# Kernel tuning notes

Measured on AMD Instinct MI355X. Metric: run time of the kernel, lower is better.

The kernel has to match this reference:

```python
import jax, jax.numpy as jnp
import numpy as np

B, T, M, D, L = 8, 4096, 32768, 128, 3  # L = ebm_GNN_layer_num - 1


def _lin(x, W, b):
    return x @ W + b


def setup_inputs() -> dict:
    key = jax.random.key(0)
    ks = jax.random.split(key, 24)
    s = 0.05
    inp = {
        "x_1st": jax.random.normal(ks[0], (B, T, 2, D), dtype=jnp.float32),
        "x_2nd": jax.random.normal(ks[1], (B, M, 4, D), dtype=jnp.float32),
        "A_causal": jax.random.uniform(ks[2], (B, 1, M), dtype=jnp.float32),
        "edge": jax.random.randint(ks[3], (2, M), 0, T, dtype=jnp.int64),
        # per-layer node/edge weights (stacked over L layers)
        "node_W": jax.random.normal(ks[4], (L, D, D)) * s,
        "node_b": jnp.zeros((L, D)),
        "mlp_W": jax.random.normal(ks[5], (L, D, D)) * s,
        "mlp_b": jnp.zeros((L, D)),
        "edgeL_W": jax.random.normal(ks[6], (L, D, D)) * s,
        "edgeL_b": jnp.zeros((L, D)),
        # node readout MLP: D -> 2D -> D -> 1
        "nro_W1": jax.random.normal(ks[7], (D, 2 * D)) * s, "nro_b1": jnp.zeros((2 * D,)),
        "nro_W2": jax.random.normal(ks[8], (2 * D, D)) * s, "nro_b2": jnp.zeros((D,)),
        "nro_W3": jax.random.normal(ks[9], (D, 1)) * s, "nro_b3": jnp.zeros((1,)),
        # edge readout MLP
        "ero_W1": jax.random.normal(ks[10], (D, 2 * D)) * s, "ero_b1": jnp.zeros((2 * D,)),
        "ero_W2": jax.random.normal(ks[11], (2 * D, D)) * s, "ero_b2": jnp.zeros((D,)),
        "ero_W3": jax.random.normal(ks[12], (D, 1)) * s, "ero_b3": jnp.zeros((1,)),
    }
    return inp


def reference(x_1st, x_2nd, A_causal, node_W, node_b, mlp_W, mlp_b,
              edgeL_W, edgeL_b, nro_W1, nro_b1, nro_W2, nro_b2, nro_W3, nro_b3,
              ero_W1, ero_b1, ero_W2, ero_b2, ero_W3, ero_b3, edge):
    ni = jnp.array([0, 0, 1, 1])  # node_i_indice
    nj = jnp.array([0, 1, 0, 1])  # node_j_indice
    e0, e1 = edge[0], edge[1]
    a = A_causal[:, 0, :, None, None]  # (B, M, 1, 1)
    xn, xe = x_1st, x_2nd
    for i in range(L):
        # --- node layer: gather -> mask-multiply -> scatter_add -> linear ---
        msg = xn[:, e1] * a                          # (B, M, 2, D)
        upd = jnp.zeros_like(xn).at[:, e0].add(msg)  # (B, T, 2, D)
        xn_new = _lin(xn + upd, node_W[i], node_b[i])
        # --- edge layer (uses updated node features, as in torch forward) ---
        ei = xn_new[:, e0][:, :, ni]                 # (B, M, 4, D)
        ej = xn_new[:, e1][:, :, nj]                 # (B, M, 4, D)
        xe_new = _lin(xe + _lin(ei + ej, mlp_W[i], mlp_b[i]), edgeL_W[i], edgeL_b[i])
        if i < L - 1:
            xn_new = jax.nn.relu(xn_new)
            xe_new = jax.nn.relu(xe_new)
        xn, xe = xn_new, xe_new
    # readouts (dropout=0, concat=False)
    h_node = _lin(jax.nn.relu(_lin(jax.nn.relu(_lin(xn, nro_W1, nro_b1)), nro_W2, nro_b2)), nro_W3, nro_b3)[..., 0]
    h_edge = _lin(jax.nn.relu(_lin(jax.nn.relu(_lin(xe, ero_W1, ero_b1)), ero_W2, ero_b2)), ero_W3, ero_b3)[..., 0]
    return h_node, h_edge  # (B,T,2), (B,M,4)
```

## Files before the change

kernel.cpp:

```cpp
#include <hip/hip_runtime.h>

#define NB 8
#define NT 4096
#define NM 32768
#define ND 128

typedef __attribute__((ext_vector_type(8))) short bf16x8;
typedef __attribute__((ext_vector_type(4))) float f32x4;
typedef __attribute__((ext_vector_type(4))) unsigned int u32x4;
typedef __attribute__((ext_vector_type(2))) unsigned int u32x2;

#define MFMA(a,b,c) __builtin_amdgcn_mfma_f32_16x16x32_bf16(a,b,c,0,0,0)

__device__ __forceinline__ unsigned short f2bf(float x) {
  unsigned u = __float_as_uint(x);
  u += 0x7FFFu + ((u >> 16) & 1u);
  return (unsigned short)(u >> 16);
}
__device__ __forceinline__ float bf2f(unsigned short h) {
  return __uint_as_float(((unsigned)h) << 16);
}
__device__ __forceinline__ u32x2 pack4bf(float a, float b, float c, float d) {
  u32x2 r;
  r[0] = ((unsigned)f2bf(b) << 16) | f2bf(a);
  r[1] = ((unsigned)f2bf(d) << 16) | f2bf(c);
  return r;
}

__device__ __forceinline__ bf16x8 ldsFrag(const char* lds, int row, int kByte, int rowStride) {
  return *(const bf16x8*)(lds + ((row * rowStride + kByte) ^ ((row & 7) << 4)));
}

__global__ __launch_bounds__(256) void k_prep(
    const float* __restrict__ W, char* __restrict__ dst,
    int K, int N, int khShift, int perShift, int total)
{
  int i = blockIdx.x * 256 + threadIdx.x;
  if (i >= total) return;
  int m  = i >> perShift;
  int j  = i & ((1 << perShift) - 1);
  int n  = j >> khShift;
  int kh = j & ((1 << khShift) - 1);
  int k0 = kh << 3;
  const float* Wm = W + (size_t)m * K * N;
  char* dm = dst + (size_t)m * K * N * 2;
  unsigned short tmp[8];
  #pragma unroll
  for (int jj = 0; jj < 8; ++jj) tmp[jj] = f2bf(Wm[(k0 + jj) * N + n]);
  *(u32x4*)(dm + ((n * K * 2 + k0 * 2) ^ ((n & 7) << 4))) = *(u32x4*)tmp;
}

__global__ __launch_bounds__(256) void k_csr_count(const int* __restrict__ edge, int* deg) {
  int m = blockIdx.x * 256 + threadIdx.x;
  if (m < NM) atomicAdd(&deg[edge[m]], 1);
}
__global__ __launch_bounds__(64) void k_csr_scan(const int* __restrict__ deg,
                                                 int* __restrict__ off, int* __restrict__ cursor) {
  __shared__ int partial[64];
  int t = threadIdx.x;
  int base = t * 64;
  int sum = 0;
  for (int i = 0; i < 64; ++i) sum += deg[base + i];
  partial[t] = sum;
  __syncthreads();
  if (t == 0) {
    int run = 0;
    for (int i = 0; i < 64; ++i) { int v = partial[i]; partial[i] = run; run += v; }
  }
  __syncthreads();
  int run = partial[t];
  for (int i = 0; i < 64; ++i) {
    off[base + i] = run; cursor[base + i] = run;
    run += deg[base + i];
  }
  if (t == 63) off[NT] = NM;
}
__global__ __launch_bounds__(256) void k_csr_fill(const int* __restrict__ edge,
                                                  int* cursor, int* __restrict__ csr) {
  int m = blockIdx.x * 256 + threadIdx.x;
  if (m < NM) { int pos = atomicAdd(&cursor[edge[m]], 1); csr[pos] = m; }
}
__global__ __launch_bounds__(256) void k_csr_sort(const int* __restrict__ off, int* __restrict__ csr) {
  int n = blockIdx.x * 256 + threadIdx.x;
  if (n < NT) {
    int s = off[n], e = off[n + 1];
    for (int i = s + 1; i < e; ++i) {
      int v = csr[i]; int j = i - 1;
      while (j >= s && csr[j] > v) { csr[j + 1] = csr[j]; --j; }
      csr[j + 1] = v;
    }
  }
}

__global__ __launch_bounds__(256, 4) void k_node(
    const float* __restrict__ xnIn, float* __restrict__ xnOut,
    const float* __restrict__ A, const int* __restrict__ edge,
    const int* __restrict__ off, const int* __restrict__ csr,
    const char* __restrict__ WImg, const float* __restrict__ bias,
    int doReluIn, int nTiles)
{
  __shared__ __align__(16) char WT[128 * 256];
  __shared__ __align__(16) char xs[32 * 256];
  const int t = threadIdx.x;
  {
    const u32x4* s = (const u32x4*)WImg;
    u32x4* d = (u32x4*)WT;
    for (int i = t; i < 2048; i += 256) d[i] = s[i];
  }
  const int w   = t >> 6;
  const int l   = t & 63;
  const int l15 = l & 15;
  const int lg  = l >> 4;
  float4 bv4[2];
  #pragma unroll
  for (int fc = 0; fc < 2; ++fc)
    bv4[fc] = *(const float4*)(bias + w * 32 + fc * 16 + lg * 4);
  const int gr = t >> 3;
  const int c0 = (t & 7) << 4;
  __syncthreads();

  for (int tile = blockIdx.x; tile < nTiles; tile += gridDim.x) {
    const int rowBase = tile << 5;
    {
      const int grow = rowBase + gr;
      const int ch   = grow & 1;
      const int node = (grow >> 1) & (NT - 1);
      const int b    = grow >> 13;
      f32x4 acc[4];
      {
        const float4* xr = (const float4*)(xnIn + (size_t)grow * ND + c0);
        #pragma unroll
        for (int q = 0; q < 4; ++q) {
          float4 v = xr[q];
          if (doReluIn) {
            v.x = fmaxf(v.x, 0.f); v.y = fmaxf(v.y, 0.f);
            v.z = fmaxf(v.z, 0.f); v.w = fmaxf(v.w, 0.f);
          }
          acc[q] = (f32x4){v.x, v.y, v.z, v.w};
        }
      }
      const int s = off[node], e = off[node + 1];
      for (int p = s; p < e; ++p) {
        int m = csr[p];
        float a = A[b * NM + m];
        int e1 = edge[NM + m];
        const float4* src = (const float4*)(xnIn + (size_t)(((b * NT + e1) << 1) + ch) * ND + c0);
        #pragma unroll
        for (int q = 0; q < 4; ++q) {
          float4 v = src[q];
          if (doReluIn) {
            v.x = fmaxf(v.x, 0.f); v.y = fmaxf(v.y, 0.f);
            v.z = fmaxf(v.z, 0.f); v.w = fmaxf(v.w, 0.f);
          }
          acc[q][0] = fmaf(a, v.x, acc[q][0]);
          acc[q][1] = fmaf(a, v.y, acc[q][1]);
          acc[q][2] = fmaf(a, v.z, acc[q][2]);
          acc[q][3] = fmaf(a, v.w, acc[q][3]);
        }
      }
      unsigned short tmp[8];
      #pragma unroll
      for (int q = 0; q < 2; ++q)
        #pragma unroll
        for (int j = 0; j < 4; ++j) tmp[q * 4 + j] = f2bf(acc[q][j]);
      *(u32x4*)(xs + ((gr * 256 + c0 * 2) ^ ((gr & 7) << 4))) = *(u32x4*)tmp;
      #pragma unroll
      for (int q = 0; q < 2; ++q)
        #pragma unroll
        for (int j = 0; j < 4; ++j) tmp[q * 4 + j] = f2bf(acc[2 + q][j]);
      *(u32x4*)(xs + ((gr * 256 + c0 * 2 + 16) ^ ((gr & 7) << 4))) = *(u32x4*)tmp;
    }
    __syncthreads();
    f32x4 acc2[2][2];
    #pragma unroll
    for (int fr = 0; fr < 2; ++fr)
      #pragma unroll
      for (int fc = 0; fc < 2; ++fc) acc2[fr][fc] = (f32x4){0.f, 0.f, 0.f, 0.f};
    #pragma unroll
    for (int ks = 0; ks < 4; ++ks) {
      int kb = ks * 64 + lg * 16;
      bf16x8 b0 = ldsFrag(WT, w * 32 + l15,      kb, 256);
      bf16x8 b1 = ldsFrag(WT, w * 32 + 16 + l15, kb, 256);
      bf16x8 a0 = ldsFrag(xs, l15,      kb, 256);
      bf16x8 a1 = ldsFrag(xs, 16 + l15, kb, 256);
      acc2[0][0] = MFMA(b0, a0, acc2[0][0]);
      acc2[0][1] = MFMA(b1, a0, acc2[0][1]);
      acc2[1][0] = MFMA(b0, a1, acc2[1][0]);
      acc2[1][1] = MFMA(b1, a1, acc2[1][1]);
    }
    __syncthreads();
    #pragma unroll
    for (int fr = 0; fr < 2; ++fr)
      #pragma unroll
      for (int fc = 0; fc < 2; ++fc) {
        int row = rowBase + fr * 16 + l15;
        int col0 = w * 32 + fc * 16 + lg * 4;
        float4 o;
        o.x = acc2[fr][fc][0] + bv4[fc].x;
        o.y = acc2[fr][fc][1] + bv4[fc].y;
        o.z = acc2[fr][fc][2] + bv4[fc].z;
        o.w = acc2[fr][fc][3] + bv4[fc].w;
        *(float4*)&xnOut[(size_t)row * ND + col0] = o;
      }
  }
}

template<int IN_F32>
__global__ __launch_bounds__(512, 2) void k_edge_mfma(
    const float* __restrict__ xn,
    const float* __restrict__ xeInF, const unsigned short* __restrict__ xeInH,
    unsigned short* xeOut,
    const int* __restrict__ edge,
    const char* __restrict__ WmImg, const float* __restrict__ bm,
    const char* __restrict__ WeImg, const float* __restrict__ be,
    int doReluOut, int nTiles)
{
  __shared__ __align__(16) char sA[64 * 256];
  __shared__ __align__(16) char sB[64 * 256];
  const int t = threadIdx.x;
  const int w   = t >> 6;
  const int l   = t & 63;
  const int l15 = l & 15;
  const int lg  = l >> 4;
  const int rg2 = w >> 2;
  const int wc  = w & 3;
  bf16x8 wmf[4][2], wef[4][2];
  #pragma unroll
  for (int ks = 0; ks < 4; ++ks)
    #pragma unroll
    for (int fc = 0; fc < 2; ++fc) {
      int n = wc * 32 + fc * 16 + l15;
      int kb = ks * 64 + lg * 16;
      wmf[ks][fc] = *(const bf16x8*)(WmImg + ((n * 256 + kb) ^ ((n & 7) << 4)));
      wef[ks][fc] = *(const bf16x8*)(WeImg + ((n * 256 + kb) ^ ((n & 7) << 4)));
    }
  float4 bmv[2], bev[2];
  #pragma unroll
  for (int fc = 0; fc < 2; ++fc) {
    int col0 = wc * 32 + fc * 16 + lg * 4;
    bmv[fc] = *(const float4*)(bm + col0);
    bev[fc] = *(const float4*)(be + col0);
  }
  const int srow = t >> 3;

  for (int tile = blockIdx.x; tile < nTiles; tile += gridDim.x) {
    const int rowBase = tile << 6;
    {
      int grow = rowBase + srow;
      int cch = grow & 3;
      int m = (grow >> 2) & (NM - 1);
      int b = grow >> 17;
      int e0 = edge[m], e1 = edge[NM + m];
      const float4* p0 = (const float4*)(xn + (size_t)((b * NT + e0) * 2 + (cch >> 1)) * ND);
      const float4* p1 = (const float4*)(xn + (size_t)((b * NT + e1) * 2 + (cch & 1)) * ND);
      #pragma unroll
      for (int hh = 0; hh < 2; ++hh) {
        int h = (t & 7) + hh * 8;
        float4 a0 = p0[h * 2], a1 = p0[h * 2 + 1];
        float4 c0 = p1[h * 2], c1 = p1[h * 2 + 1];
        unsigned short tmp[8];
        tmp[0] = f2bf(a0.x + c0.x); tmp[1] = f2bf(a0.y + c0.y);
        tmp[2] = f2bf(a0.z + c0.z); tmp[3] = f2bf(a0.w + c0.w);
        tmp[4] = f2bf(a1.x + c1.x); tmp[5] = f2bf(a1.y + c1.y);
        tmp[6] = f2bf(a1.z + c1.z); tmp[7] = f2bf(a1.w + c1.w);
        *(u32x4*)(sA + ((srow * 256 + h * 16) ^ ((srow & 7) << 4))) = *(u32x4*)tmp;
      }
    }
    float4 xev[2][2];
    #pragma unroll
    for (int fr = 0; fr < 2; ++fr)
      #pragma unroll
      for (int fc = 0; fc < 2; ++fc) {
        int row = rowBase + rg2 * 32 + fr * 16 + l15;
        int col0 = wc * 32 + fc * 16 + lg * 4;
        if (IN_F32) {
          xev[fr][fc] = *(const float4*)(xeInF + (size_t)row * ND + col0);
        } else {
          ushort4 h4 = *(const ushort4*)(xeInH + (size_t)row * ND + col0);
          xev[fr][fc] = (float4){bf2f(h4.x), bf2f(h4.y), bf2f(h4.z), bf2f(h4.w)};
        }
      }
    __syncthreads();
    f32x4 acc[2][2];
    #pragma unroll
    for (int fr = 0; fr < 2; ++fr)
      #pragma unroll
      for (int fc = 0; fc < 2; ++fc) acc[fr][fc] = (f32x4){0.f, 0.f, 0.f, 0.f};
    #pragma unroll
    for (int ks = 0; ks < 4; ++ks) {
      int kb = ks * 64 + lg * 16;
      #pragma unroll
      for (int fr = 0; fr < 2; ++fr) {
        bf16x8 a = ldsFrag(sA, rg2 * 32 + fr * 16 + l15, kb, 256);
        acc[fr][0] = MFMA(wmf[ks][0], a, acc[fr][0]);
        acc[fr][1] = MFMA(wmf[ks][1], a, acc[fr][1]);
      }
    }
    #pragma unroll
    for (int fr = 0; fr < 2; ++fr)
      #pragma unroll
      for (int fc = 0; fc < 2; ++fc) {
        int row = rg2 * 32 + fr * 16 + l15;
        int kByte = (wc * 32 + fc * 16 + lg * 4) * 2;
        u32x2 pk = pack4bf(xev[fr][fc].x + acc[fr][fc][0] + bmv[fc].x,
                           xev[fr][fc].y + acc[fr][fc][1] + bmv[fc].y,
                           xev[fr][fc].z + acc[fr][fc][2] + bmv[fc].z,
                           xev[fr][fc].w + acc[fr][fc][3] + bmv[fc].w);
        *(u32x2*)(sB + ((row * 256 + kByte) ^ ((row & 7) << 4))) = pk;
      }
    __syncthreads();
    #pragma unroll
    for (int fr = 0; fr < 2; ++fr)
      #pragma unroll
      for (int fc = 0; fc < 2; ++fc) acc[fr][fc] = (f32x4){0.f, 0.f, 0.f, 0.f};
    #pragma unroll
    for (int ks = 0; ks < 4; ++ks) {
      int kb = ks * 64 + lg * 16;
      #pragma unroll
      for (int fr = 0; fr < 2; ++fr) {
        bf16x8 a = ldsFrag(sB, rg2 * 32 + fr * 16 + l15, kb, 256);
        acc[fr][0] = MFMA(wef[ks][0], a, acc[fr][0]);
        acc[fr][1] = MFMA(wef[ks][1], a, acc[fr][1]);
      }
    }
    #pragma unroll
    for (int fr = 0; fr < 2; ++fr)
      #pragma unroll
      for (int fc = 0; fc < 2; ++fc) {
        int row = rowBase + rg2 * 32 + fr * 16 + l15;
        int col0 = wc * 32 + fc * 16 + lg * 4;
        float o0 = acc[fr][fc][0] + bev[fc].x;
        float o1 = acc[fr][fc][1] + bev[fc].y;
        float o2 = acc[fr][fc][2] + bev[fc].z;
        float o3 = acc[fr][fc][3] + bev[fc].w;
        if (doReluOut) {
          o0 = fmaxf(o0, 0.f); o1 = fmaxf(o1, 0.f);
          o2 = fmaxf(o2, 0.f); o3 = fmaxf(o3, 0.f);
        }
        u32x2 pk = pack4bf(o0, o1, o2, o3);
        *(u32x2*)(xeOut + (size_t)row * ND + col0) = pk;
      }
  }
}

template<int INBF16>
__global__ __launch_bounds__(512, 2) void k_ro_fused(
    const float* __restrict__ inF, const unsigned short* __restrict__ inH,
    float* __restrict__ out, int nTiles,
    const char* __restrict__ W1Img, const float* __restrict__ b1,
    const char* __restrict__ W2Img, const float* __restrict__ b2,
    const float* __restrict__ W3, const float* __restrict__ b3)
{
  __shared__ __align__(16) char sA[64 * 256];
  __shared__ __align__(16) char h1[64 * 512];
  __shared__ float red[2][64][8];
  const int t = threadIdx.x;
  const int w   = t >> 6;
  const int l   = t & 63;
  const int l15 = l & 15;
  const int lg  = l >> 4;
  bf16x8 w1f[4][2];
  #pragma unroll
  for (int ks = 0; ks < 4; ++ks)
    #pragma unroll
    for (int fc = 0; fc < 2; ++fc) {
      int n = w * 32 + fc * 16 + l15;
      int kb = ks * 64 + lg * 16;
      w1f[ks][fc] = *(const bf16x8*)(W1Img + ((n * 256 + kb) ^ ((n & 7) << 4)));
    }
  bf16x8 w2f[8];
  #pragma unroll
  for (int ks = 0; ks < 8; ++ks) {
    int n = w * 16 + l15;
    int kb = ks * 64 + lg * 16;
    w2f[ks] = *(const bf16x8*)(W2Img + ((n * 512 + kb) ^ ((n & 7) << 4)));
  }
  float4 b1v[2];
  #pragma unroll
  for (int fc = 0; fc < 2; ++fc)
    b1v[fc] = *(const float4*)(b1 + w * 32 + fc * 16 + lg * 4);
  const float4 b2v = *(const float4*)(b2 + w * 16 + lg * 4);
  const float4 w3v = *(const float4*)(W3 + w * 16 + lg * 4);
  const float b3v = b3[0];
  const int srow  = t >> 3;
  const int sbyte = (t & 7) << 5;
  u32x4 pvH[2];
  int tile = blockIdx.x;
  if (tile < nTiles) {
    if (INBF16) {
      const char* p = (const char*)inH + (size_t)((tile << 6) + srow) * 256 + sbyte;
      pvH[0] = *(const u32x4*)p;
      pvH[1] = *(const u32x4*)(p + 16);
    } else {
      const float4* p = (const float4*)(inF + (size_t)((tile << 6) + srow) * ND + ((t & 7) << 4));
      unsigned short tmp[16];
      #pragma unroll
      for (int q = 0; q < 4; ++q) {
        float4 v = p[q];
        tmp[q * 4 + 0] = f2bf(v.x); tmp[q * 4 + 1] = f2bf(v.y);
        tmp[q * 4 + 2] = f2bf(v.z); tmp[q * 4 + 3] = f2bf(v.w);
      }
      pvH[0] = *(u32x4*)tmp; pvH[1] = *(u32x4*)(tmp + 8);
    }
  }

  int par = 0;
  int prevRow = -1;
  for (; tile < nTiles; tile += gridDim.x) {
    const int rowBase = tile << 6;
    *(u32x4*)(sA + ((srow * 256 + sbyte) ^ ((srow & 7) << 4))) = pvH[0];
    *(u32x4*)(sA + ((srow * 256 + sbyte + 16) ^ ((srow & 7) << 4))) = pvH[1];
    __syncthreads();
    if (prevRow >= 0 && t < 64) {
      float s = b3v;
      #pragma unroll
      for (int q = 0; q < 8; ++q) s += red[par ^ 1][t][q];
      out[prevRow + t] = s;
    }
    {
      int nt2 = tile + (int)gridDim.x;
      if (nt2 < nTiles) {
        if (INBF16) {
          const char* p = (const char*)inH + (size_t)((nt2 << 6) + srow) * 256 + sbyte;
          pvH[0] = *(const u32x4*)p;
          pvH[1] = *(const u32x4*)(p + 16);
        } else {
          const float4* p = (const float4*)(inF + (size_t)((nt2 << 6) + srow) * ND + ((t & 7) << 4));
          unsigned short tmp[16];
          #pragma unroll
          for (int q = 0; q < 4; ++q) {
            float4 v = p[q];
            tmp[q * 4 + 0] = f2bf(v.x); tmp[q * 4 + 1] = f2bf(v.y);
            tmp[q * 4 + 2] = f2bf(v.z); tmp[q * 4 + 3] = f2bf(v.w);
          }
          pvH[0] = *(u32x4*)tmp; pvH[1] = *(u32x4*)(tmp + 8);
        }
      }
    }
    {
      f32x4 acc[4][2];
      #pragma unroll
      for (int fr = 0; fr < 4; ++fr)
        #pragma unroll
        for (int fc = 0; fc < 2; ++fc) acc[fr][fc] = (f32x4){0.f, 0.f, 0.f, 0.f};
      #pragma unroll
      for (int ks = 0; ks < 4; ++ks) {
        int kb = ks * 64 + lg * 16;
        #pragma unroll
        for (int fr = 0; fr < 4; ++fr) {
          bf16x8 a = ldsFrag(sA, fr * 16 + l15, kb, 256);
          acc[fr][0] = MFMA(w1f[ks][0], a, acc[fr][0]);
          acc[fr][1] = MFMA(w1f[ks][1], a, acc[fr][1]);
        }
      }
      #pragma unroll
      for (int fr = 0; fr < 4; ++fr)
        #pragma unroll
        for (int fc = 0; fc < 2; ++fc) {
          int row = fr * 16 + l15;
          int kByte = (w * 32 + fc * 16 + lg * 4) * 2;
          u32x2 pk = pack4bf(fmaxf(acc[fr][fc][0] + b1v[fc].x, 0.f),
                             fmaxf(acc[fr][fc][1] + b1v[fc].y, 0.f),
                             fmaxf(acc[fr][fc][2] + b1v[fc].z, 0.f),
                             fmaxf(acc[fr][fc][3] + b1v[fc].w, 0.f));
          *(u32x2*)(h1 + ((row * 512 + kByte) ^ ((row & 7) << 4))) = pk;
        }
    }
    __syncthreads();
    {
      f32x4 acc[4];
      #pragma unroll
      for (int fr = 0; fr < 4; ++fr) acc[fr] = (f32x4){0.f, 0.f, 0.f, 0.f};
      #pragma unroll
      for (int ks = 0; ks < 8; ++ks) {
        int kb = ks * 64 + lg * 16;
        #pragma unroll
        for (int fr = 0; fr < 4; ++fr) {
          bf16x8 a = ldsFrag(h1, fr * 16 + l15, kb, 512);
          acc[fr] = MFMA(w2f[ks], a, acc[fr]);
        }
      }
      #pragma unroll
      for (int fr = 0; fr < 4; ++fr) {
        float p = fmaxf(acc[fr][0] + b2v.x, 0.f) * w3v.x
                + fmaxf(acc[fr][1] + b2v.y, 0.f) * w3v.y
                + fmaxf(acc[fr][2] + b2v.z, 0.f) * w3v.z
                + fmaxf(acc[fr][3] + b2v.w, 0.f) * w3v.w;
        p += __shfl_xor(p, 16);
        p += __shfl_xor(p, 32);
        if (lg == 0) red[par][fr * 16 + l15][w] = p;
      }
    }
    prevRow = rowBase;
    par ^= 1;
  }
  __syncthreads();
  if (prevRow >= 0 && t < 64) {
    float s = b3v;
    #pragma unroll
    for (int q = 0; q < 8; ++q) s += red[par ^ 1][t][q];
    out[prevRow + t] = s;
  }
}

extern "C" void kernel_launch(void* const* d_in, const int* in_sizes, int n_in,
                              void* d_out, int out_size, void* d_ws, size_t ws_size,
                              hipStream_t stream)
{
  const float* x1     = (const float*)d_in[0];
  const float* x2     = (const float*)d_in[1];
  const float* Ac     = (const float*)d_in[2];
  const int*   edge   = (const int*)d_in[3];
  const float* node_W = (const float*)d_in[4];
  const float* node_b = (const float*)d_in[5];
  const float* mlp_W  = (const float*)d_in[6];
  const float* mlp_b  = (const float*)d_in[7];
  const float* egL_W  = (const float*)d_in[8];
  const float* egL_b  = (const float*)d_in[9];
  const float* nro_W1 = (const float*)d_in[10];
  const float* nro_b1 = (const float*)d_in[11];
  const float* nro_W2 = (const float*)d_in[12];
  const float* nro_b2 = (const float*)d_in[13];
  const float* nro_W3 = (const float*)d_in[14];
  const float* nro_b3 = (const float*)d_in[15];
  const float* ero_W1 = (const float*)d_in[16];
  const float* ero_b1 = (const float*)d_in[17];
  const float* ero_W2 = (const float*)d_in[18];
  const float* ero_b2 = (const float*)d_in[19];
  const float* ero_W3 = (const float*)d_in[20];
  const float* ero_b3 = (const float*)d_in[21];
  float* out = (float*)d_out;

  const size_t xnElems = (size_t)NB * NT * 2 * ND;
  const size_t xeElems = (size_t)NB * NM * 4 * ND;
  const size_t wBytes  = 3 * 128 * 128 * 2 * 3
                       + 4 * (128 * 256 * 2);
  if (ws_size < xnElems * 2 * sizeof(float) + xeElems * 2 + wBytes) return;

  float* xnA = (float*)d_ws;
  float* xnB = xnA + xnElems;
  unsigned short* xeH = (unsigned short*)(xnB + xnElems);
  char*  wWm = (char*)(xeH + xeElems);
  char*  wWe = wWm + 3 * 128 * 128 * 2;
  char*  wNd = wWe + 3 * 128 * 128 * 2;
  char*  wN1 = wNd + 3 * 128 * 128 * 2;
  char*  wN2 = wN1 + 128 * 256 * 2;
  char*  wE1 = wN2 + 128 * 256 * 2;
  char*  wE2 = wE1 + 128 * 256 * 2;

  int* deg    = (int*)d_out;
  int* off    = deg + NT;
  int* cursor = off + NT + 1;
  int* csr    = cursor + NT;

  k_prep<<<24, 256, 0, stream>>>(mlp_W, wWm, 128, 128, 4, 11, 3 * 2048);
  k_prep<<<24, 256, 0, stream>>>(egL_W, wWe, 128, 128, 4, 11, 3 * 2048);
  k_prep<<<24, 256, 0, stream>>>(node_W, wNd, 128, 128, 4, 11, 3 * 2048);
  k_prep<<<16, 256, 0, stream>>>(nro_W1, wN1, 128, 256, 4, 12, 4096);
  k_prep<<<16, 256, 0, stream>>>(nro_W2, wN2, 256, 128, 5, 12, 4096);
  k_prep<<<16, 256, 0, stream>>>(ero_W1, wE1, 128, 256, 4, 12, 4096);
  k_prep<<<16, 256, 0, stream>>>(ero_W2, wE2, 256, 128, 5, 12, 4096);

  hipMemsetAsync(deg, 0, NT * sizeof(int), stream);
  k_csr_count<<<NM / 256, 256, 0, stream>>>(edge, deg);
  k_csr_scan<<<1, 64, 0, stream>>>(deg, off, cursor);
  k_csr_fill<<<NM / 256, 256, 0, stream>>>(edge, cursor, csr);
  k_csr_sort<<<NT / 256, 256, 0, stream>>>(off, csr);

  const int eTiles = (NB * NM * 4) / 64;
  const int nTilesN = (NB * NT * 2) / 32;
  k_node<<<1024, 256, 0, stream>>>(x1, xnA, Ac, edge, off, csr, wNd, node_b, 0, nTilesN);
  k_edge_mfma<1><<<512, 512, 0, stream>>>(xnA, x2, nullptr, xeH, edge,
                                          wWm, mlp_b, wWe, egL_b, 1, eTiles);
  k_node<<<1024, 256, 0, stream>>>(xnA, xnB, Ac, edge, off, csr,
                                   wNd + 128 * 128 * 2, node_b + ND, 1, nTilesN);
  k_edge_mfma<0><<<512, 512, 0, stream>>>(xnB, nullptr, xeH, xeH, edge,
                                          wWm + 128 * 128 * 2, mlp_b + ND,
                                          wWe + 128 * 128 * 2, egL_b + ND, 1, eTiles);
  k_node<<<1024, 256, 0, stream>>>(xnB, xnA, Ac, edge, off, csr,
                                   wNd + 2 * 128 * 128 * 2, node_b + 2 * ND, 1, nTilesN);
  k_edge_mfma<0><<<512, 512, 0, stream>>>(xnA, nullptr, xeH, xeH, edge,
                                          wWm + 2 * 128 * 128 * 2, mlp_b + 2 * ND,
                                          wWe + 2 * 128 * 128 * 2, egL_b + 2 * ND, 0, eTiles);
  k_ro_fused<0><<<512, 512, 0, stream>>>(xnA, nullptr, out, (NB * NT * 2) / 64,
                                         wN1, nro_b1, wN2, nro_b2, nro_W3, nro_b3);
  k_ro_fused<1><<<512, 512, 0, stream>>>(nullptr, xeH, out + NB * NT * 2, (NB * NM * 4) / 64,
                                         wE1, ero_b1, wE2, ero_b2, ero_W3, ero_b3);
}
```

Measured before the change: 1.232 ms.

## Reorder layers and split edge pipeline into cache-resident halves

Runs all three node layers first into three separate node buffers, since node updates do not depend on edge features. The three edge layers and the edge readout then run back-to-back on each half of the edge tiles, so the intermediate bf16 edge features for one half can stay resident in the last-level cache between kernels. This cuts HBM traffic for the repeated edge-feature reads and writes. The cost is twice as many launches with smaller per-launch work, plus an extra node-feature workspace buffer.

```diff
diff --git a/kernel.cpp b/kernel.cpp
--- a/kernel.cpp
+++ b/kernel.cpp
@@ -213,7 +213,7 @@
     const int* __restrict__ edge,
     const char* __restrict__ WmImg, const float* __restrict__ bm,
     const char* __restrict__ WeImg, const float* __restrict__ be,
-    int doReluOut, int nTiles)
+    int doReluOut, int tileStart, int tileEnd)
 {
   __shared__ __align__(16) char sA[64 * 256];
   __shared__ __align__(16) char sB[64 * 256];
@@ -243,7 +243,7 @@
   }
   const int srow = t >> 3;
 
-  for (int tile = blockIdx.x; tile < nTiles; tile += gridDim.x) {
+  for (int tile = tileStart + blockIdx.x; tile < tileEnd; tile += gridDim.x) {
     const int rowBase = tile << 6;
     {
       int grow = rowBase + srow;
@@ -346,7 +346,7 @@
 template<int INBF16>
 __global__ __launch_bounds__(512, 2) void k_ro_fused(
     const float* __restrict__ inF, const unsigned short* __restrict__ inH,
-    float* __restrict__ out, int nTiles,
+    float* __restrict__ out, int tileStart, int tileEnd,
     const char* __restrict__ W1Img, const float* __restrict__ b1,
     const char* __restrict__ W2Img, const float* __restrict__ b2,
     const float* __restrict__ W3, const float* __restrict__ b3)
@@ -385,8 +385,8 @@
   const int srow  = t >> 3;
   const int sbyte = (t & 7) << 5;
   u32x4 pvH[2];
-  int tile = blockIdx.x;
-  if (tile < nTiles) {
+  int tile = tileStart + blockIdx.x;
+  if (tile < tileEnd) {
     if (INBF16) {
       const char* p = (const char*)inH + (size_t)((tile << 6) + srow) * 256 + sbyte;
       pvH[0] = *(const u32x4*)p;
@@ -406,7 +406,7 @@
 
   int par = 0;
   int prevRow = -1;
-  for (; tile < nTiles; tile += gridDim.x) {
+  for (; tile < tileEnd; tile += gridDim.x) {
     const int rowBase = tile << 6;
     *(u32x4*)(sA + ((srow * 256 + sbyte) ^ ((srow & 7) << 4))) = pvH[0];
     *(u32x4*)(sA + ((srow * 256 + sbyte + 16) ^ ((srow & 7) << 4))) = pvH[1];
@@ -419,7 +419,7 @@
     }
     {
       int nt2 = tile + (int)gridDim.x;
-      if (nt2 < nTiles) {
+      if (nt2 < tileEnd) {
         if (INBF16) {
           const char* p = (const char*)inH + (size_t)((nt2 << 6) + srow) * 256 + sbyte;
           pvH[0] = *(const u32x4*)p;
@@ -535,11 +535,12 @@
   const size_t xeElems = (size_t)NB * NM * 4 * ND;
   const size_t wBytes  = 3 * 128 * 128 * 2 * 3
                        + 4 * (128 * 256 * 2);
-  if (ws_size < xnElems * 2 * sizeof(float) + xeElems * 2 + wBytes) return;
-
-  float* xnA = (float*)d_ws;
-  float* xnB = xnA + xnElems;
-  unsigned short* xeH = (unsigned short*)(xnB + xnElems);
+  if (ws_size < xnElems * 3 * sizeof(float) + xeElems * 2 + wBytes) return;
+
+  float* xn0 = (float*)d_ws;
+  float* xn1 = xn0 + xnElems;
+  float* xn2 = xn1 + xnElems;
+  unsigned short* xeH = (unsigned short*)(xn2 + xnElems);
   char*  wWm = (char*)(xeH + xeElems);
   char*  wWe = wWm + 3 * 128 * 128 * 2;
   char*  wNd = wWe + 3 * 128 * 128 * 2;
@@ -567,23 +568,28 @@
   k_csr_fill<<<NM / 256, 256, 0, stream>>>(edge, cursor, csr);
   k_csr_sort<<<NT / 256, 256, 0, stream>>>(off, csr);
 
+  const int nTilesN = (NB * NT * 2) / 32;
+  k_node<<<1024, 256, 0, stream>>>(x1, xn0, Ac, edge, off, csr, wNd, node_b, 0, nTilesN);
+  k_node<<<1024, 256, 0, stream>>>(xn0, xn1, Ac, edge, off, csr,
+                                   wNd + 128 * 128 * 2, node_b + ND, 1, nTilesN);
+  k_node<<<1024, 256, 0, stream>>>(xn1, xn2, Ac, edge, off, csr,
+                                   wNd + 2 * 128 * 128 * 2, node_b + 2 * ND, 1, nTilesN);
+
   const int eTiles = (NB * NM * 4) / 64;
-  const int nTilesN = (NB * NT * 2) / 32;
-  k_node<<<1024, 256, 0, stream>>>(x1, xnA, Ac, edge, off, csr, wNd, node_b, 0, nTilesN);
-  k_edge_mfma<1><<<512, 512, 0, stream>>>(xnA, x2, nullptr, xeH, edge,
-                                          wWm, mlp_b, wWe, egL_b, 1, eTiles);
-  k_node<<<1024, 256, 0, stream>>>(xnA, xnB, Ac, edge, off, csr,
-                                   wNd + 128 * 128 * 2, node_b + ND, 1, nTilesN);
-  k_edge_mfma<0><<<512, 512, 0, stream>>>(xnB, nullptr, xeH, xeH, edge,
-                                          wWm + 128 * 128 * 2, mlp_b + ND,
-                                          wWe + 128 * 128 * 2, egL_b + ND, 1, eTiles);
-  k_node<<<1024, 256, 0, stream>>>(xnB, xnA, Ac, edge, off, csr,
-                                   wNd + 2 * 128 * 128 * 2, node_b + 2 * ND, 1, nTilesN);
-  k_edge_mfma<0><<<512, 512, 0, stream>>>(xnA, nullptr, xeH, xeH, edge,
-                                          wWm + 2 * 128 * 128 * 2, mlp_b + 2 * ND,
-                                          wWe + 2 * 128 * 128 * 2, egL_b + 2 * ND, 0, eTiles);
-  k_ro_fused<0><<<512, 512, 0, stream>>>(xnA, nullptr, out, (NB * NT * 2) / 64,
+  const int half = eTiles / 2;
+  for (int bb = 0; bb < 2; ++bb) {
+    int ts = bb * half, te = ts + half;
+    k_edge_mfma<1><<<512, 512, 0, stream>>>(xn0, x2, nullptr, xeH, edge,
+                                            wWm, mlp_b, wWe, egL_b, 1, ts, te);
+    k_edge_mfma<0><<<512, 512, 0, stream>>>(xn1, nullptr, xeH, xeH, edge,
+                                            wWm + 128 * 128 * 2, mlp_b + ND,
+                                            wWe + 128 * 128 * 2, egL_b + ND, 1, ts, te);
+    k_edge_mfma<0><<<512, 512, 0, stream>>>(xn2, nullptr, xeH, xeH, edge,
+                                            wWm + 2 * 128 * 128 * 2, mlp_b + 2 * ND,
+                                            wWe + 2 * 128 * 128 * 2, egL_b + 2 * ND, 0, ts, te);
+    k_ro_fused<1><<<512, 512, 0, stream>>>(nullptr, xeH, out + NB * NT * 2, ts, te,
+                                           wE1, ero_b1, wE2, ero_b2, ero_W3, ero_b3);
+  }
+  k_ro_fused<0><<<512, 512, 0, stream>>>(xn2, nullptr, out, 0, (NB * NT * 2) / 64,
                                          wN1, nro_b1, wN2, nro_b2, nro_W3, nro_b3);
-  k_ro_fused<1><<<512, 512, 0, stream>>>(nullptr, xeH, out + NB * NT * 2, (NB * NM * 4) / 64,
-                                         wE1, ero_b1, wE2, ero_b2, ero_W3, ero_b3);
-}
+}
```

New measurement: 1.227 ms. About the same (-0.4%).
